# Optimization experiments

Hardware: AMD Instinct MI355X
Metric: run time of the kernel (lower is better)

## Reference

```python
import jax, jax.numpy as jnp
import numpy as np

N_NODES = 50000
N_EDGES = 640000
HID = 128


def _lin_params(key, out_dim, in_dim):
    kw, kb = jax.random.split(key)
    W = jax.random.normal(kw, (out_dim, in_dim), dtype=jnp.float32) * 0.02
    b = jax.random.normal(kb, (out_dim,), dtype=jnp.float32) * 0.02
    return W, b


def setup_inputs() -> dict:
    key = jax.random.key(0)
    ks = jax.random.split(key, 12)
    x = jax.random.normal(ks[0], (N_NODES, 3), dtype=jnp.float32)
    h = jax.random.normal(ks[1], (N_NODES, HID), dtype=jnp.float32)
    edge_index = jax.random.randint(ks[2], (2, N_EDGES), 0, N_NODES, dtype=jnp.int64)
    # edge_mlp: Linear(2H+1,H) -> SiLU -> Linear(H,H) -> SiLU -> Linear(H,H)
    ew1, eb1 = _lin_params(ks[3], HID, 2 * HID + 1)
    ew2, eb2 = _lin_params(ks[4], HID, HID)
    ew3, eb3 = _lin_params(ks[5], HID, HID)
    # coord_mlp: Linear(H,H) -> SiLU -> Linear(H,1)
    cw1, cb1 = _lin_params(ks[6], HID, HID)
    cw2, cb2 = _lin_params(ks[7], 1, HID)
    # node_mlp: Linear(2H,H) -> SiLU -> Linear(H,H) -> SiLU -> Linear(H,H)
    nw1, nb1 = _lin_params(ks[8], HID, 2 * HID)
    nw2, nb2 = _lin_params(ks[9], HID, HID)
    nw3, nb3 = _lin_params(ks[10], HID, HID)
    return {
        "x": x, "h": h, "edge_index": edge_index,
        "ew1": ew1, "eb1": eb1, "ew2": ew2, "eb2": eb2, "ew3": ew3, "eb3": eb3,
        "cw1": cw1, "cb1": cb1, "cw2": cw2, "cb2": cb2,
        "nw1": nw1, "nb1": nb1, "nw2": nw2, "nb2": nb2, "nw3": nw3, "nb3": nb3,
    }


def _lin(z, W, b):
    return z @ W.T + b


def _mlp3(z, W1, b1, W2, b2, W3, b3):
    z = jax.nn.silu(_lin(z, W1, b1))
    z = jax.nn.silu(_lin(z, W2, b2))
    return _lin(z, W3, b3)


def reference(x, h, edge_index,
              ew1, eb1, ew2, eb2, ew3, eb3,
              cw1, cb1, cw2, cb2,
              nw1, nb1, nw2, nb2, nw3, nb3):
    n = h.shape[0]
    src, dst = edge_index[0], edge_index[1]
    rel = x[src] - x[dst]                                   # [E, 3]
    d2 = jnp.sum(rel * rel, axis=-1, keepdims=True)         # [E, 1]
    e_in = jnp.concatenate([h[src], h[dst], d2], axis=-1)   # [E, 2H+1]
    m_ij = _mlp3(e_in, ew1, eb1, ew2, eb2, ew3, eb3)        # [E, H]
    m_aggr = jax.ops.segment_sum(m_ij, src, num_segments=n)  # [N, H]
    coord_coef = jnp.tanh(_lin(jax.nn.silu(_lin(m_ij, cw1, cb1)), cw2, cb2))  # [E, 1]
    delta_x = jax.ops.segment_sum(rel * coord_coef, src, num_segments=n)      # [N, 3]
    x_out = x + delta_x
    h_out = h + _mlp3(jnp.concatenate([h, m_aggr], axis=-1), nw1, nb1, nw2, nb2, nw3, nb3)
    return (x_out, h_out)
```

## Files before the change

### kernel.cpp

```cpp
#include <hip/hip_runtime.h>
#include <hip/hip_bf16.h>

#define N_NODES 50000
#define N_EDGES 640000
#define HID 128
#define EDG 128

typedef unsigned short ushort_t;
typedef __attribute__((ext_vector_type(8))) short bf16x8;
typedef __attribute__((ext_vector_type(4))) float f32x4;

#define U_MAGGR 0
#define U_HB    6400000
#define U_W1B   12800000
#define U_W2B   12832768
#define U_W3B   12849152
#define U_C1B   12865536
#define U_N1B   12881920
#define U_N2B   12914688
#define U_N3B   12931072
#define U_W1D2  12947456
#define U_WC    12947712
#define U_BC    12964096
#define U_SD    12964352
#define U_CNT   15524352
#define U_PTR   15624448

__device__ __forceinline__ float silu_f(float v) {
    const float e = __builtin_amdgcn_exp2f(v * -1.442695041f);
    return v * __builtin_amdgcn_rcpf(1.0f + e);
}

__device__ __forceinline__ ushort_t f2b(float f) {
    __hip_bfloat16 b = __float2bfloat16(f);
    return __builtin_bit_cast(ushort_t, b);
}
__device__ __forceinline__ float b2f(ushort_t u) {
    union { float f; unsigned int i; } v; v.i = ((unsigned int)u) << 16; return v.f;
}
__device__ __forceinline__ float u2f(unsigned int u) {
    union { float f; unsigned int i; } v; v.i = u; return v.f;
}
__device__ __forceinline__ unsigned int pack2(float a, float b) {
    return (unsigned int)f2b(a) | ((unsigned int)f2b(b) << 16);
}
__device__ __forceinline__ void up8(const uint4& u, float* f) {
    f[0] = u2f(u.x << 16); f[1] = u2f(u.x & 0xffff0000u);
    f[2] = u2f(u.y << 16); f[3] = u2f(u.y & 0xffff0000u);
    f[4] = u2f(u.z << 16); f[5] = u2f(u.z & 0xffff0000u);
    f[6] = u2f(u.w << 16); f[7] = u2f(u.w & 0xffff0000u);
}
__device__ __forceinline__ void atom_add_f32(float* p, float v) { unsafeAtomicAdd(p, v); }

__device__ __forceinline__ void atom_pk_bf16(ushort_t* p, unsigned int v) {
#if __has_builtin(__builtin_amdgcn_global_atomic_fadd_v2bf16)
    typedef __attribute__((ext_vector_type(2))) short s2;
    s2 sv = __builtin_bit_cast(s2, v);
    __builtin_amdgcn_global_atomic_fadd_v2bf16((__attribute__((address_space(1))) s2*)p, sv);
#else
    unsigned int* up = (unsigned int*)p;
    unsigned int old = __hip_atomic_load(up, __ATOMIC_RELAXED, __HIP_MEMORY_SCOPE_AGENT), assumed;
    do {
        assumed = old;
        float lo = b2f((ushort_t)(assumed & 0xffff)) + b2f((ushort_t)(v & 0xffff));
        float hi = b2f((ushort_t)(assumed >> 16)) + b2f((ushort_t)(v >> 16));
        unsigned int nv = (unsigned int)f2b(lo) | ((unsigned int)f2b(hi) << 16);
        old = atomicCAS(up, assumed, nv);
    } while (old != assumed);
#endif
}

__global__ void prep_kernel(const float* __restrict__ x, const float* __restrict__ h,
                            const float* __restrict__ ew1, const float* __restrict__ ew2,
                            const float* __restrict__ ew3, const float* __restrict__ cw1,
                            const float* __restrict__ nw1, const float* __restrict__ nw2,
                            const float* __restrict__ nw3, const int* __restrict__ ei,
                            ushort_t* __restrict__ wsu, float* __restrict__ xout) {
    long i = (long)blockIdx.x * 256 + threadIdx.x;
    if (i < 800000) {
        ((uint4*)(wsu + U_MAGGR))[i] = make_uint4(0u, 0u, 0u, 0u);
        return;
    }
    i -= 800000;
    if (i < 800000) {
        const float4* h4 = (const float4*)h;
        const float4 f0 = h4[2 * i], f1 = h4[2 * i + 1];
        ((uint4*)(wsu + U_HB))[i] = make_uint4(pack2(f0.x, f0.y), pack2(f0.z, f0.w),
                                               pack2(f1.x, f1.y), pack2(f1.z, f1.w));
        return;
    }
    i -= 800000;
    if (i < 32768) {
        const int f = (int)(i >> 7);
        const int k = (int)(i & 127);
        const int src = (f < 128) ? (f * 257 + k) : ((f - 128) * 257 + 128 + k);
        wsu[U_W1B + i] = f2b(ew1[src]);
        return;
    }
    i -= 32768;
    if (i < 16384) { wsu[U_W2B + i] = f2b(ew2[i]); return; }
    i -= 16384;
    if (i < 16384) { wsu[U_W3B + i] = f2b(ew3[i]); return; }
    i -= 16384;
    if (i < 16384) { wsu[U_C1B + i] = f2b(cw1[i]); return; }
    i -= 16384;
    if (i < 32768) { wsu[U_N1B + i] = f2b(nw1[i]); return; }
    i -= 32768;
    if (i < 16384) { wsu[U_N2B + i] = f2b(nw2[i]); return; }
    i -= 16384;
    if (i < 16384) { wsu[U_N3B + i] = f2b(nw3[i]); return; }
    i -= 16384;
    if (i < 128) { ((float*)(wsu + U_W1D2))[i] = ew1[i * 257 + 256]; return; }
    i -= 128;
    if (i < 37500) { ((float4*)xout)[i] = ((const float4*)x)[i]; return; }
    i -= 37500;
    if (i < N_EDGES) {
        atomicAdd(((unsigned int*)(wsu + U_CNT)) + ei[i], 1u);
    }
}

__global__ void scatter_kernel(const int* __restrict__ ei, unsigned int* __restrict__ ptr,
                               int2* __restrict__ sd) {
    const int e = blockIdx.x * 256 + threadIdx.x;
    if (e >= N_EDGES) return;
    const int s = ei[e], d = ei[N_EDGES + e];
    const unsigned int pos = atomicAdd(&ptr[s], 1u);
    sd[pos] = make_int2(s, d);
}

__global__ __launch_bounds__(256, 4) void ab_kernel(
    const ushort_t* __restrict__ hb, const ushort_t* __restrict__ wab,
    const float* __restrict__ eb1, ushort_t* __restrict__ abp,
    const ushort_t* __restrict__ c1b, const float* __restrict__ ew3,
    const float* __restrict__ eb3, const float* __restrict__ cb1,
    ushort_t* __restrict__ wcb, float* __restrict__ bcv,
    const unsigned int* __restrict__ cnt, unsigned int* __restrict__ ptr, int nAB) {
    __shared__ ushort_t sH[16384];
    const int t = threadIdx.x;
    const int lane = t & 63;
    const int wid = t >> 6;
    const int r15 = lane & 15;
    const int khi = lane >> 4;
    const int rhi = khi * 4;

    if ((int)blockIdx.x == nAB + 1) {
        __shared__ unsigned int sSum[256];
        const int lo = t * 196;
        const int hi = (lo + 196 < N_NODES) ? lo + 196 : N_NODES;
        unsigned int s = 0;
#pragma unroll 4
        for (int i = lo; i < hi; ++i) s += cnt[i];
        sSum[t] = s;
        __syncthreads();
#pragma unroll
        for (int off = 1; off < 256; off <<= 1) {
            const unsigned int v = (t >= off) ? sSum[t - off] : 0u;
            __syncthreads();
            sSum[t] += v;
            __syncthreads();
        }
        unsigned int run = (t == 0) ? 0u : sSum[t - 1];
#pragma unroll 4
        for (int i = lo; i < hi; ++i) { const unsigned int c = cnt[i]; ptr[i] = run; run += c; }
        return;
    }

    if ((int)blockIdx.x == nAB) {
        for (int i = t; i < 16384; i += 256) {
            const int m = i >> 7, k = i & 127;
            sH[(k * 128 + m) ^ ((k & 7) << 3)] = f2b(ew3[i]);
        }
        __syncthreads();
#pragma unroll
        for (int kh = 0; kh < 2; ++kh) {
#pragma unroll
            for (int fi = 0; fi < 2; ++fi) {
                const int f0 = wid * 32 + fi * 16;
                const int kc = kh * 64;
                f32x4 acc[4];
#pragma unroll
                for (int ni = 0; ni < 4; ++ni) acc[ni] = (f32x4){0.f, 0.f, 0.f, 0.f};
#pragma unroll
                for (int ks = 0; ks < 4; ++ks) {
                    const bf16x8 a0 = *(const bf16x8*)(c1b + (f0 + r15) * 128 + ks * 32 + khi * 8);
                    bf16x8 b[4];
#pragma unroll
                    for (int ni = 0; ni < 4; ++ni) {
                        const int kk = kc + ni * 16 + r15;
                        b[ni] = *(const bf16x8*)(sH + ((kk * 128 + ks * 32 + khi * 8) ^ ((kk & 7) << 3)));
                    }
#pragma unroll
                    for (int ni = 0; ni < 4; ++ni)
                        acc[ni] = __builtin_amdgcn_mfma_f32_16x16x32_bf16(a0, b[ni], acc[ni], 0, 0, 0);
                }
#pragma unroll
                for (int ni = 0; ni < 4; ++ni) {
                    const int kk = kc + ni * 16 + r15;
#pragma unroll
                    for (int j = 0; j < 4; ++j)
                        wcb[(f0 + rhi + j) * 128 + kk] = f2b(acc[ni][j]);
                }
            }
        }
        {
            const int f = t >> 1, hf = t & 1;
            float s = 0.f;
            const int m0 = hf * 64;
#pragma unroll 8
            for (int m = m0; m < m0 + 64; ++m)
                s = fmaf(b2f(c1b[f * 128 + m]), eb3[m], s);
            s += __shfl_xor(s, 1);
            if (hf == 0) bcv[f] = cb1[f] + s;
        }
        return;
    }

    const int fb = wid * 64;
    const int n0 = blockIdx.x * 64;

    const uint4* hb4 = (const uint4*)hb;
#pragma unroll
    for (int it = 0; it < 4; ++it) {
        const int idx = it * 256 + t;
        const int e = idx >> 4, c = idx & 15;
        const int n = n0 + e;
        uint4 v = make_uint4(0u, 0u, 0u, 0u);
        if (n < N_NODES) v = hb4[(size_t)n * 16 + c];
        const int ui = (e * 128 + c * 8) ^ ((e & 7) << 3);
        *(uint4*)(sH + ui) = v;
    }
    __syncthreads();

    f32x4 acc[4][4];
#pragma unroll
    for (int mi = 0; mi < 4; ++mi)
#pragma unroll
        for (int ni = 0; ni < 4; ++ni) acc[mi][ni] = (f32x4){0.f, 0.f, 0.f, 0.f};
#pragma unroll
    for (int ks = 0; ks < 4; ++ks) {
        bf16x8 a[4];
#pragma unroll
        for (int mi = 0; mi < 4; ++mi)
            a[mi] = *(const bf16x8*)(wab + (fb + mi * 16 + r15) * 128 + ks * 32 + khi * 8);
        bf16x8 b[4];
#pragma unroll
        for (int ni = 0; ni < 4; ++ni) {
            const int e = ni * 16 + r15;
            const int ui = (e * 128 + ks * 32 + khi * 8) ^ ((e & 7) << 3);
            b[ni] = *(const bf16x8*)(sH + ui);
        }
#pragma unroll
        for (int mi = 0; mi < 4; ++mi)
#pragma unroll
            for (int ni = 0; ni < 4; ++ni)
                acc[mi][ni] = __builtin_amdgcn_mfma_f32_16x16x32_bf16(a[mi], b[ni], acc[mi][ni], 0, 0, 0);
    }

#pragma unroll
    for (int mi = 0; mi < 4; ++mi) {
        const int f0 = fb + mi * 16 + rhi;
        float4 bb = make_float4(0.f, 0.f, 0.f, 0.f);
        if (f0 >= 128) bb = *(const float4*)&eb1[f0 - 128];
#pragma unroll
        for (int ni = 0; ni < 4; ++ni) {
            const int n = n0 + ni * 16 + r15;
            if (n < N_NODES) {
                *(uint2*)(abp + (size_t)n * 256 + f0) =
                    make_uint2(pack2(acc[mi][ni][0] + bb.x, acc[mi][ni][1] + bb.y),
                               pack2(acc[mi][ni][2] + bb.z, acc[mi][ni][3] + bb.w));
            }
        }
    }
}

template <bool ACT, int NE>
__device__ __forceinline__ void dense128(ushort_t* sE, int srcBase, int dstBase,
                                         const ushort_t* __restrict__ W,
                                         const float* __restrict__ bias,
                                         int r15, int khi, int rhi, int fb) {
    f32x4 acc[NE];
#pragma unroll
    for (int ni = 0; ni < NE; ++ni) acc[ni] = (f32x4){0.f, 0.f, 0.f, 0.f};
#pragma unroll
    for (int ks = 0; ks < 4; ++ks) {
        const bf16x8 a0 = *(const bf16x8*)(W + (fb + r15) * 128 + ks * 32 + khi * 8);
        bf16x8 b[NE];
#pragma unroll
        for (int ni = 0; ni < NE; ++ni) {
            const int edge = ni * 16 + r15;
            const int ui = (srcBase + edge * 128 + ks * 32 + khi * 8) ^ ((edge & 7) << 3);
            b[ni] = *(const bf16x8*)(sE + ui);
        }
#pragma unroll
        for (int ni = 0; ni < NE; ++ni)
            acc[ni] = __builtin_amdgcn_mfma_f32_16x16x32_bf16(a0, b[ni], acc[ni], 0, 0, 0);
    }
    const float4 bb = *(const float4*)&bias[fb + rhi];
#pragma unroll
    for (int ni = 0; ni < NE; ++ni) {
        const int edge = ni * 16 + r15;
        float v0 = acc[ni][0] + bb.x;
        float v1 = acc[ni][1] + bb.y;
        float v2 = acc[ni][2] + bb.z;
        float v3 = acc[ni][3] + bb.w;
        if (ACT) { v0 = silu_f(v0); v1 = silu_f(v1); v2 = silu_f(v2); v3 = silu_f(v3); }
        const int ui = (dstBase + edge * 128 + fb + rhi) ^ ((edge & 7) << 3);
        *(uint2*)(sE + ui) = make_uint2(pack2(v0, v1), pack2(v2, v3));
    }
}

__global__ __launch_bounds__(512, 4) void edge_kernel(
    const float* __restrict__ x, const ushort_t* __restrict__ ab,
    const int2* __restrict__ sd,
    const float* __restrict__ w1d2,
    const ushort_t* __restrict__ w2b, const float* __restrict__ eb2,
    const ushort_t* __restrict__ w3b, const float* __restrict__ eb3,
    const ushort_t* __restrict__ wcb, const float* __restrict__ bcv,
    const float* __restrict__ cw2, const float* __restrict__ cb2,
    float* __restrict__ xout, ushort_t* __restrict__ maggr) {
    __shared__ ushort_t sE[32768];
    __shared__ float srel[EDG][3];
    __shared__ float sd2[EDG];
    __shared__ int ssrc[EDG];
    __shared__ float sPart[8][EDG];

    const int t = threadIdx.x;
    const int lane = t & 63;
    const int wid = t >> 6;
    const int r15 = lane & 15;
    const int khi = lane >> 4;
    const int rhi = khi * 4;
    const int fb = wid * 16;
    const int e0 = blockIdx.x * EDG;

    uint4 va[4], vb[4];
    const int c = t & 15;
    const int ebase = t >> 4;
    {
        const uint4* ab4 = (const uint4*)ab;
#pragma unroll
        for (int it = 0; it < 4; ++it) {
            const int e = it * 32 + ebase;
            const int2 p = sd[e0 + e];
            va[it] = ab4[(size_t)p.x * 32 + c];
            vb[it] = ab4[(size_t)p.y * 32 + 16 + c];
        }
    }
    if (t < EDG) {
        const int2 p = sd[e0 + t];
        ssrc[t] = p.x;
        const float rx = x[3 * p.x] - x[3 * p.y];
        const float ry = x[3 * p.x + 1] - x[3 * p.y + 1];
        const float rz = x[3 * p.x + 2] - x[3 * p.y + 2];
        srel[t][0] = rx; srel[t][1] = ry; srel[t][2] = rz;
        sd2[t] = rx * rx + ry * ry + rz * rz;
    }
    __syncthreads();

    {
        const float4 w0 = *(const float4*)&w1d2[c * 8];
        const float4 w1 = *(const float4*)&w1d2[c * 8 + 4];
#pragma unroll
        for (int it = 0; it < 4; ++it) {
            const int e = it * 32 + ebase;
            const float d2 = sd2[e];
            float fa[8], fbv[8];
            up8(va[it], fa);
            up8(vb[it], fbv);
            const float v0 = silu_f(fmaf(d2, w0.x, fa[0] + fbv[0]));
            const float v1 = silu_f(fmaf(d2, w0.y, fa[1] + fbv[1]));
            const float v2 = silu_f(fmaf(d2, w0.z, fa[2] + fbv[2]));
            const float v3 = silu_f(fmaf(d2, w0.w, fa[3] + fbv[3]));
            const float v4 = silu_f(fmaf(d2, w1.x, fa[4] + fbv[4]));
            const float v5 = silu_f(fmaf(d2, w1.y, fa[5] + fbv[5]));
            const float v6 = silu_f(fmaf(d2, w1.z, fa[6] + fbv[6]));
            const float v7 = silu_f(fmaf(d2, w1.w, fa[7] + fbv[7]));
            uint4 st;
            st.x = pack2(v0, v1); st.y = pack2(v2, v3);
            st.z = pack2(v4, v5); st.w = pack2(v6, v7);
            *(uint4*)(sE + ((e * 128 + c * 8) ^ ((e & 7) << 3))) = st;
        }
    }
    __syncthreads();

    dense128<true, EDG / 16>(sE, 0, 16384, w2b, eb2, r15, khi, rhi, fb);
    __syncthreads();

    dense128<false, EDG / 16>(sE, 16384, 0, w3b, eb3, r15, khi, rhi, fb);

    {
        f32x4 acc[EDG / 16];
#pragma unroll
        for (int ni = 0; ni < EDG / 16; ++ni) acc[ni] = (f32x4){0.f, 0.f, 0.f, 0.f};
#pragma unroll
        for (int ks = 0; ks < 4; ++ks) {
            const bf16x8 a0 = *(const bf16x8*)(wcb + (fb + r15) * 128 + ks * 32 + khi * 8);
            bf16x8 b[EDG / 16];
#pragma unroll
            for (int ni = 0; ni < EDG / 16; ++ni) {
                const int edge = ni * 16 + r15;
                const int u = (16384 + edge * 128 + ks * 32 + khi * 8) ^ ((edge & 7) << 3);
                b[ni] = *(const bf16x8*)(sE + u);
            }
#pragma unroll
            for (int ni = 0; ni < EDG / 16; ++ni)
                acc[ni] = __builtin_amdgcn_mfma_f32_16x16x32_bf16(a0, b[ni], acc[ni], 0, 0, 0);
        }
        const float4 bb = *(const float4*)&bcv[fb + rhi];
        const float4 cw = *(const float4*)&cw2[fb + rhi];
        float p[EDG / 16];
#pragma unroll
        for (int ni = 0; ni < EDG / 16; ++ni) {
            float s = silu_f(acc[ni][0] + bb.x) * cw.x;
            s = fmaf(silu_f(acc[ni][1] + bb.y), cw.y, s);
            s = fmaf(silu_f(acc[ni][2] + bb.z), cw.z, s);
            s = fmaf(silu_f(acc[ni][3] + bb.w), cw.w, s);
            p[ni] = s;
        }
#pragma unroll
        for (int ni = 0; ni < EDG / 16; ++ni) {
            p[ni] += __shfl_xor(p[ni], 16);
            p[ni] += __shfl_xor(p[ni], 32);
        }
        if (khi == 0) {
#pragma unroll
            for (int ni = 0; ni < EDG / 16; ++ni) sPart[wid][ni * 16 + r15] = p[ni];
        }
    }
    __syncthreads();

    if (t < EDG) {
        float s = sPart[0][t];
#pragma unroll
        for (int w = 1; w < 8; ++w) s += sPart[w][t];
        const float coef = tanhf(s + cb2[0]);
        sPart[0][t] = srel[t][0] * coef;
        sPart[1][t] = srel[t][1] * coef;
        sPart[2][t] = srel[t][2] * coef;
    }

    {
        const int dw = t & 63;
        const int rs = t >> 6;
        float lo = 0.f, hi = 0.f;
        int cur = ssrc[rs * 16];
#pragma unroll
        for (int j = 0; j < 16; ++j) {
            const int e = rs * 16 + j;
            const int s = ssrc[e];
            if (s != cur) {
                atom_pk_bf16(maggr + (size_t)cur * 128 + dw * 2, pack2(lo, hi));
                lo = 0.f; hi = 0.f; cur = s;
            }
            const unsigned int v = *(const unsigned int*)(sE + ((e * 128 + dw * 2) ^ ((e & 7) << 3)));
            lo += b2f((ushort_t)(v & 0xffff));
            hi += b2f((ushort_t)(v >> 16));
        }
        atom_pk_bf16(maggr + (size_t)cur * 128 + dw * 2, pack2(lo, hi));
    }
    __syncthreads();

    if (t < EDG) {
        const bool last = (t == EDG - 1) || (ssrc[t + 1] != ssrc[t]);
        if (last) {
            const int s = ssrc[t];
            float ax = 0.f, ay = 0.f, az = 0.f;
            int j = t;
            while (j >= 0 && ssrc[j] == s) {
                ax += sPart[0][j]; ay += sPart[1][j]; az += sPart[2][j];
                --j;
            }
            atom_add_f32(&xout[3 * s + 0], ax);
            atom_add_f32(&xout[3 * s + 1], ay);
            atom_add_f32(&xout[3 * s + 2], az);
        }
    }
}

__global__ __launch_bounds__(256, 4) void node_kernel(
    const float* __restrict__ h, const ushort_t* __restrict__ hb,
    const ushort_t* __restrict__ maggr,
    const ushort_t* __restrict__ n1b, const float* __restrict__ nb1,
    const ushort_t* __restrict__ n2b, const float* __restrict__ nb2,
    const ushort_t* __restrict__ n3b, const float* __restrict__ nb3,
    float* __restrict__ hout) {
    __shared__ ushort_t sE[16384];
    const int t = threadIdx.x;
    const int lane = t & 63;
    const int wid = t >> 6;
    const int r15 = lane & 15;
    const int khi = lane >> 4;
    const int rhi = khi * 4;
    const int fb = wid * 32;
    const int n0 = blockIdx.x * 64;

    const uint4* hb4 = (const uint4*)hb;
    const uint4* mg4 = (const uint4*)maggr;
#pragma unroll
    for (int it = 0; it < 8; ++it) {
        const int idx = it * 256 + t;
        const int e = idx >> 5, c = idx & 31;
        const int n = n0 + e;
        uint4 v = make_uint4(0u, 0u, 0u, 0u);
        if (n < N_NODES) v = (c < 16) ? hb4[(size_t)n * 16 + c] : mg4[(size_t)n * 16 + (c - 16)];
        const int ui = (e * 256 + c * 8) ^ ((e & 7) << 3);
        *(uint4*)(sE + ui) = v;
    }
    __syncthreads();

    f32x4 acc[2][4];
#pragma unroll
    for (int mi = 0; mi < 2; ++mi)
#pragma unroll
        for (int ni = 0; ni < 4; ++ni) acc[mi][ni] = (f32x4){0.f, 0.f, 0.f, 0.f};
#pragma unroll
    for (int ks = 0; ks < 8; ++ks) {
        const bf16x8 a0 = *(const bf16x8*)(n1b + (fb + r15) * 256 + ks * 32 + khi * 8);
        const bf16x8 a1 = *(const bf16x8*)(n1b + (fb + 16 + r15) * 256 + ks * 32 + khi * 8);
        bf16x8 b[4];
#pragma unroll
        for (int ni = 0; ni < 4; ++ni) {
            const int edge = ni * 16 + r15;
            const int ui = (edge * 256 + ks * 32 + khi * 8) ^ ((edge & 7) << 3);
            b[ni] = *(const bf16x8*)(sE + ui);
        }
#pragma unroll
        for (int ni = 0; ni < 4; ++ni) {
            acc[0][ni] = __builtin_amdgcn_mfma_f32_16x16x32_bf16(a0, b[ni], acc[0][ni], 0, 0, 0);
            acc[1][ni] = __builtin_amdgcn_mfma_f32_16x16x32_bf16(a1, b[ni], acc[1][ni], 0, 0, 0);
        }
    }
    __syncthreads();
    {
        const float4 bb0 = *(const float4*)&nb1[fb + rhi];
        const float4 bb1 = *(const float4*)&nb1[fb + 16 + rhi];
#pragma unroll
        for (int mi = 0; mi < 2; ++mi) {
            const float4 bb = mi ? bb1 : bb0;
#pragma unroll
            for (int ni = 0; ni < 4; ++ni) {
                const int edge = ni * 16 + r15;
                const float v0 = silu_f(acc[mi][ni][0] + bb.x);
                const float v1 = silu_f(acc[mi][ni][1] + bb.y);
                const float v2 = silu_f(acc[mi][ni][2] + bb.z);
                const float v3 = silu_f(acc[mi][ni][3] + bb.w);
                const int ui = (edge * 128 + fb + mi * 16 + rhi) ^ ((edge & 7) << 3);
                *(uint2*)(sE + ui) = make_uint2(pack2(v0, v1), pack2(v2, v3));
            }
        }
    }
    __syncthreads();

    {
#pragma unroll
        for (int half = 0; half < 2; ++half) {
            f32x4 a2[4];
#pragma unroll
            for (int ni = 0; ni < 4; ++ni) a2[ni] = (f32x4){0.f, 0.f, 0.f, 0.f};
            const int fbh = fb + half * 16;
#pragma unroll
            for (int ks = 0; ks < 4; ++ks) {
                const bf16x8 a0 = *(const bf16x8*)(n2b + (fbh + r15) * 128 + ks * 32 + khi * 8);
                bf16x8 b[4];
#pragma unroll
                for (int ni = 0; ni < 4; ++ni) {
                    const int edge = ni * 16 + r15;
                    const int ui = (edge * 128 + ks * 32 + khi * 8) ^ ((edge & 7) << 3);
                    b[ni] = *(const bf16x8*)(sE + ui);
                }
#pragma unroll
                for (int ni = 0; ni < 4; ++ni)
                    a2[ni] = __builtin_amdgcn_mfma_f32_16x16x32_bf16(a0, b[ni], a2[ni], 0, 0, 0);
            }
            const float4 bb = *(const float4*)&nb2[fbh + rhi];
#pragma unroll
            for (int ni = 0; ni < 4; ++ni) {
                const int edge = ni * 16 + r15;
                const float v0 = silu_f(a2[ni][0] + bb.x);
                const float v1 = silu_f(a2[ni][1] + bb.y);
                const float v2 = silu_f(a2[ni][2] + bb.z);
                const float v3 = silu_f(a2[ni][3] + bb.w);
                const int ui = (8192 + edge * 128 + fbh + rhi) ^ ((edge & 7) << 3);
                *(uint2*)(sE + ui) = make_uint2(pack2(v0, v1), pack2(v2, v3));
            }
        }
    }
    __syncthreads();

    {
        f32x4 a3[2][4];
#pragma unroll
        for (int mi = 0; mi < 2; ++mi)
#pragma unroll
            for (int ni = 0; ni < 4; ++ni) a3[mi][ni] = (f32x4){0.f, 0.f, 0.f, 0.f};
#pragma unroll
        for (int ks = 0; ks < 4; ++ks) {
            const bf16x8 a0 = *(const bf16x8*)(n3b + (fb + r15) * 128 + ks * 32 + khi * 8);
            const bf16x8 a1 = *(const bf16x8*)(n3b + (fb + 16 + r15) * 128 + ks * 32 + khi * 8);
            bf16x8 b[4];
#pragma unroll
            for (int ni = 0; ni < 4; ++ni) {
                const int edge = ni * 16 + r15;
                const int ui = (8192 + edge * 128 + ks * 32 + khi * 8) ^ ((edge & 7) << 3);
                b[ni] = *(const bf16x8*)(sE + ui);
            }
#pragma unroll
            for (int ni = 0; ni < 4; ++ni) {
                a3[0][ni] = __builtin_amdgcn_mfma_f32_16x16x32_bf16(a0, b[ni], a3[0][ni], 0, 0, 0);
                a3[1][ni] = __builtin_amdgcn_mfma_f32_16x16x32_bf16(a1, b[ni], a3[1][ni], 0, 0, 0);
            }
        }
        const float4 bb0 = *(const float4*)&nb3[fb + rhi];
        const float4 bb1 = *(const float4*)&nb3[fb + 16 + rhi];
#pragma unroll
        for (int mi = 0; mi < 2; ++mi) {
            const float4 bb = mi ? bb1 : bb0;
#pragma unroll
            for (int ni = 0; ni < 4; ++ni) {
                const int n = n0 + ni * 16 + r15;
                if (n < N_NODES) {
                    const size_t o = (size_t)n * 128 + fb + mi * 16 + rhi;
                    const float4 hv = *(const float4*)&h[o];
                    float4 ov;
                    ov.x = hv.x + a3[mi][ni][0] + bb.x;
                    ov.y = hv.y + a3[mi][ni][1] + bb.y;
                    ov.z = hv.z + a3[mi][ni][2] + bb.z;
                    ov.w = hv.w + a3[mi][ni][3] + bb.w;
                    *(float4*)&hout[o] = ov;
                }
            }
        }
    }
}

extern "C" void kernel_launch(void* const* d_in, const int* in_sizes, int n_in,
                              void* d_out, int out_size, void* d_ws, size_t ws_size,
                              hipStream_t stream) {
    const float* x   = (const float*)d_in[0];
    const float* h   = (const float*)d_in[1];
    const int*   ei  = (const int*)d_in[2];
    const float* ew1 = (const float*)d_in[3];
    const float* eb1 = (const float*)d_in[4];
    const float* ew2 = (const float*)d_in[5];
    const float* eb2 = (const float*)d_in[6];
    const float* ew3 = (const float*)d_in[7];
    const float* eb3 = (const float*)d_in[8];
    const float* cw1 = (const float*)d_in[9];
    const float* cb1 = (const float*)d_in[10];
    const float* cw2 = (const float*)d_in[11];
    const float* cb2 = (const float*)d_in[12];
    const float* nw1 = (const float*)d_in[13];
    const float* nb1 = (const float*)d_in[14];
    const float* nw2 = (const float*)d_in[15];
    const float* nb2 = (const float*)d_in[16];
    const float* nw3 = (const float*)d_in[17];
    const float* nb3 = (const float*)d_in[18];

    float* out  = (float*)d_out;
    float* xout = out;
    float* hout = out + (size_t)N_NODES * 3;
    ushort_t* wsu = (ushort_t*)d_ws;

    ushort_t* maggr = wsu + U_MAGGR;
    const ushort_t* hb  = wsu + U_HB;
    const ushort_t* wab = wsu + U_W1B;
    const ushort_t* w2b = wsu + U_W2B;
    const ushort_t* w3b = wsu + U_W3B;
    const ushort_t* c1b = wsu + U_C1B;
    const ushort_t* n1b = wsu + U_N1B;
    const ushort_t* n2b = wsu + U_N2B;
    const ushort_t* n3b = wsu + U_N3B;
    const float* w1d2 = (const float*)(wsu + U_W1D2);
    ushort_t* wcb = wsu + U_WC;
    float* bcv = (float*)(wsu + U_BC);
    int2* sd = (int2*)(wsu + U_SD);
    unsigned int* cnt = (unsigned int*)(wsu + U_CNT);
    unsigned int* ptr = (unsigned int*)(wsu + U_PTR);

    ushort_t* abp = (ushort_t*)hout;

    hipMemsetAsync(cnt, 0, 50048 * sizeof(unsigned int), stream);

    const long prep_total = 800000L + 800000L + 32768 + 3 * 16384 + 32768 + 2 * 16384 + 128 + 37500 + N_EDGES;
    const int prep_blocks = (int)((prep_total + 255) / 256);
    prep_kernel<<<prep_blocks, 256, 0, stream>>>(x, h, ew1, ew2, ew3, cw1, nw1, nw2, nw3,
                                                 ei, wsu, xout);

    const int nAB = (N_NODES + 63) / 64;
    ab_kernel<<<nAB + 2, 256, 0, stream>>>(hb, wab, eb1, abp,
                                           c1b, ew3, eb3, cb1, wcb, bcv,
                                           cnt, ptr, nAB);

    scatter_kernel<<<(N_EDGES + 255) / 256, 256, 0, stream>>>(ei, ptr, sd);

    edge_kernel<<<N_EDGES / EDG, 512, 0, stream>>>(x, abp, sd,
                                                   w1d2, w2b, eb2, w3b, eb3,
                                                   wcb, bcv, cw2, cb2,
                                                   xout, maggr);

    node_kernel<<<(N_NODES + 63) / 64, 256, 0, stream>>>(h, hb, maggr,
                                                         n1b, nb1, n2b, nb2, n3b, nb3,
                                                         hout);
}
```

Baseline: 321.2 us.

## Retile edge MLP to 32x64 warp tiles and fuse scatter into AB kernel

The edge kernel's dense layers now give each warp a 32-feature by 64-edge tile instead of a 16-feature by 128-edge tile. Each B fragment read from LDS then feeds two MFMAs, which halves LDS traffic per MFMA, and the coord partial sums reduce over 4 slots instead of 8. Separately, the prefix scan moves into its own 1024-thread kernel. The edge scatter runs as extra blocks of the AB GEMM kernel, which removes a launch and lets the scatter overlap with the GEMM. The costs are a serial single-block scan launch beforehand and higher register pressure per warp.

```diff
diff --git a/kernel.cpp b/kernel.cpp
--- a/kernel.cpp
+++ b/kernel.cpp
@@ -119,51 +119,53 @@
     }
 }
 
-__global__ void scatter_kernel(const int* __restrict__ ei, unsigned int* __restrict__ ptr,
-                               int2* __restrict__ sd) {
-    const int e = blockIdx.x * 256 + threadIdx.x;
-    if (e >= N_EDGES) return;
-    const int s = ei[e], d = ei[N_EDGES + e];
-    const unsigned int pos = atomicAdd(&ptr[s], 1u);
-    sd[pos] = make_int2(s, d);
-}
-
-__global__ __launch_bounds__(256, 4) void ab_kernel(
+__global__ __launch_bounds__(1024) void scan_kernel(const unsigned int* __restrict__ cnt,
+                                                    unsigned int* __restrict__ ptr) {
+    __shared__ unsigned int sSum[1024];
+    const int t = threadIdx.x;
+    const int lo = t * 49;
+    const int hi = (lo + 49 < N_NODES) ? lo + 49 : N_NODES;
+    unsigned int s = 0;
+    for (int i = lo; i < hi; ++i) s += cnt[i];
+    sSum[t] = s;
+    __syncthreads();
+#pragma unroll
+    for (int off = 1; off < 1024; off <<= 1) {
+        const unsigned int v = (t >= off) ? sSum[t - off] : 0u;
+        __syncthreads();
+        sSum[t] += v;
+        __syncthreads();
+    }
+    unsigned int run = (t == 0) ? 0u : sSum[t - 1];
+    for (int i = lo; i < hi; ++i) { const unsigned int c = cnt[i]; ptr[i] = run; run += c; }
+}
+
+__global__ __launch_bounds__(256, 4) void abscatter_kernel(
     const ushort_t* __restrict__ hb, const ushort_t* __restrict__ wab,
     const float* __restrict__ eb1, ushort_t* __restrict__ abp,
     const ushort_t* __restrict__ c1b, const float* __restrict__ ew3,
     const float* __restrict__ eb3, const float* __restrict__ cb1,
     ushort_t* __restrict__ wcb, float* __restrict__ bcv,
-    const unsigned int* __restrict__ cnt, unsigned int* __restrict__ ptr, int nAB) {
+    const int* __restrict__ ei, unsigned int* __restrict__ ptr, int2* __restrict__ sd,
+    int nAB) {
     __shared__ ushort_t sH[16384];
     const int t = threadIdx.x;
+
+    if ((int)blockIdx.x > nAB) {
+        const int e = ((int)blockIdx.x - nAB - 1) * 256 + t;
+        if (e < N_EDGES) {
+            const int s = ei[e], d = ei[N_EDGES + e];
+            const unsigned int pos = atomicAdd(&ptr[s], 1u);
+            sd[pos] = make_int2(s, d);
+        }
+        return;
+    }
+
     const int lane = t & 63;
     const int wid = t >> 6;
     const int r15 = lane & 15;
     const int khi = lane >> 4;
     const int rhi = khi * 4;
-
-    if ((int)blockIdx.x == nAB + 1) {
-        __shared__ unsigned int sSum[256];
-        const int lo = t * 196;
-        const int hi = (lo + 196 < N_NODES) ? lo + 196 : N_NODES;
-        unsigned int s = 0;
-#pragma unroll 4
-        for (int i = lo; i < hi; ++i) s += cnt[i];
-        sSum[t] = s;
-        __syncthreads();
-#pragma unroll
-        for (int off = 1; off < 256; off <<= 1) {
-            const unsigned int v = (t >= off) ? sSum[t - off] : 0u;
-            __syncthreads();
-            sSum[t] += v;
-            __syncthreads();
-        }
-        unsigned int run = (t == 0) ? 0u : sSum[t - 1];
-#pragma unroll 4
-        for (int i = lo; i < hi; ++i) { const unsigned int c = cnt[i]; ptr[i] = run; run += c; }
-        return;
-    }
 
     if ((int)blockIdx.x == nAB) {
         for (int i = t; i < 16384; i += 256) {
@@ -273,39 +275,49 @@
     }
 }
 
-template <bool ACT, int NE>
-__device__ __forceinline__ void dense128(ushort_t* sE, int srcBase, int dstBase,
-                                         const ushort_t* __restrict__ W,
-                                         const float* __restrict__ bias,
-                                         int r15, int khi, int rhi, int fb) {
-    f32x4 acc[NE];
-#pragma unroll
-    for (int ni = 0; ni < NE; ++ni) acc[ni] = (f32x4){0.f, 0.f, 0.f, 0.f};
+template <bool ACT>
+__device__ __forceinline__ void dense32x64(ushort_t* sE, int srcBase, int dstBase,
+                                           const ushort_t* __restrict__ W,
+                                           const float* __restrict__ bias,
+                                           int r15, int khi, int rhi, int fb, int eb) {
+    f32x4 acc[2][4];
+#pragma unroll
+    for (int mi = 0; mi < 2; ++mi)
+#pragma unroll
+        for (int ni = 0; ni < 4; ++ni) acc[mi][ni] = (f32x4){0.f, 0.f, 0.f, 0.f};
 #pragma unroll
     for (int ks = 0; ks < 4; ++ks) {
         const bf16x8 a0 = *(const bf16x8*)(W + (fb + r15) * 128 + ks * 32 + khi * 8);
-        bf16x8 b[NE];
-#pragma unroll
-        for (int ni = 0; ni < NE; ++ni) {
-            const int edge = ni * 16 + r15;
+        const bf16x8 a1 = *(const bf16x8*)(W + (fb + 16 + r15) * 128 + ks * 32 + khi * 8);
+        bf16x8 b[4];
+#pragma unroll
+        for (int ni = 0; ni < 4; ++ni) {
+            const int edge = eb + ni * 16 + r15;
             const int ui = (srcBase + edge * 128 + ks * 32 + khi * 8) ^ ((edge & 7) << 3);
             b[ni] = *(const bf16x8*)(sE + ui);
         }
 #pragma unroll
-        for (int ni = 0; ni < NE; ++ni)
-            acc[ni] = __builtin_amdgcn_mfma_f32_16x16x32_bf16(a0, b[ni], acc[ni], 0, 0, 0);
-    }
-    const float4 bb = *(const float4*)&bias[fb + rhi];
-#pragma unroll
-    for (int ni = 0; ni < NE; ++ni) {
-        const int edge = ni * 16 + r15;
-        float v0 = acc[ni][0] + bb.x;
-        float v1 = acc[ni][1] + bb.y;
-        float v2 = acc[ni][2] + bb.z;
-        float v3 = acc[ni][3] + bb.w;
-        if (ACT) { v0 = silu_f(v0); v1 = silu_f(v1); v2 = silu_f(v2); v3 = silu_f(v3); }
-        const int ui = (dstBase + edge * 128 + fb + rhi) ^ ((edge & 7) << 3);
-        *(uint2*)(sE + ui) = make_uint2(pack2(v0, v1), pack2(v2, v3));
+        for (int ni = 0; ni < 4; ++ni) {
+            acc[0][ni] = __builtin_amdgcn_mfma_f32_16x16x32_bf16(a0, b[ni], acc[0][ni], 0, 0, 0);
+            acc[1][ni] = __builtin_amdgcn_mfma_f32_16x16x32_bf16(a1, b[ni], acc[1][ni], 0, 0, 0);
+        }
+    }
+    const float4 bb0 = *(const float4*)&bias[fb + rhi];
+    const float4 bb1 = *(const float4*)&bias[fb + 16 + rhi];
+#pragma unroll
+    for (int mi = 0; mi < 2; ++mi) {
+        const float4 bb = mi ? bb1 : bb0;
+#pragma unroll
+        for (int ni = 0; ni < 4; ++ni) {
+            const int edge = eb + ni * 16 + r15;
+            float v0 = acc[mi][ni][0] + bb.x;
+            float v1 = acc[mi][ni][1] + bb.y;
+            float v2 = acc[mi][ni][2] + bb.z;
+            float v3 = acc[mi][ni][3] + bb.w;
+            if (ACT) { v0 = silu_f(v0); v1 = silu_f(v1); v2 = silu_f(v2); v3 = silu_f(v3); }
+            const int ui = (dstBase + edge * 128 + fb + mi * 16 + rhi) ^ ((edge & 7) << 3);
+            *(uint2*)(sE + ui) = make_uint2(pack2(v0, v1), pack2(v2, v3));
+        }
     }
 }
 
@@ -322,7 +334,7 @@
     __shared__ float srel[EDG][3];
     __shared__ float sd2[EDG];
     __shared__ int ssrc[EDG];
-    __shared__ float sPart[8][EDG];
+    __shared__ float sPart[4][EDG];
 
     const int t = threadIdx.x;
     const int lane = t & 63;
@@ -330,7 +342,10 @@
     const int r15 = lane & 15;
     const int khi = lane >> 4;
     const int rhi = khi * 4;
-    const int fb = wid * 16;
+    const int fg = wid & 3;
+    const int eh = wid >> 2;
+    const int fb = fg * 32;
+    const int eb = eh * 64;
     const int e0 = blockIdx.x * EDG;
 
     uint4 va[4], vb[4];
@@ -383,56 +398,65 @@
     }
     __syncthreads();
 
-    dense128<true, EDG / 16>(sE, 0, 16384, w2b, eb2, r15, khi, rhi, fb);
-    __syncthreads();
-
-    dense128<false, EDG / 16>(sE, 16384, 0, w3b, eb3, r15, khi, rhi, fb);
+    dense32x64<true>(sE, 0, 16384, w2b, eb2, r15, khi, rhi, fb, eb);
+    __syncthreads();
+
+    dense32x64<false>(sE, 16384, 0, w3b, eb3, r15, khi, rhi, fb, eb);
 
     {
-        f32x4 acc[EDG / 16];
-#pragma unroll
-        for (int ni = 0; ni < EDG / 16; ++ni) acc[ni] = (f32x4){0.f, 0.f, 0.f, 0.f};
+        f32x4 acc[2][4];
+#pragma unroll
+        for (int mi = 0; mi < 2; ++mi)
+#pragma unroll
+            for (int ni = 0; ni < 4; ++ni) acc[mi][ni] = (f32x4){0.f, 0.f, 0.f, 0.f};
 #pragma unroll
         for (int ks = 0; ks < 4; ++ks) {
             const bf16x8 a0 = *(const bf16x8*)(wcb + (fb + r15) * 128 + ks * 32 + khi * 8);
-            bf16x8 b[EDG / 16];
-#pragma unroll
-            for (int ni = 0; ni < EDG / 16; ++ni) {
-                const int edge = ni * 16 + r15;
+            const bf16x8 a1 = *(const bf16x8*)(wcb + (fb + 16 + r15) * 128 + ks * 32 + khi * 8);
+            bf16x8 b[4];
+#pragma unroll
+            for (int ni = 0; ni < 4; ++ni) {
+                const int edge = eb + ni * 16 + r15;
                 const int u = (16384 + edge * 128 + ks * 32 + khi * 8) ^ ((edge & 7) << 3);
                 b[ni] = *(const bf16x8*)(sE + u);
             }
 #pragma unroll
-            for (int ni = 0; ni < EDG / 16; ++ni)
-                acc[ni] = __builtin_amdgcn_mfma_f32_16x16x32_bf16(a0, b[ni], acc[ni], 0, 0, 0);
-        }
-        const float4 bb = *(const float4*)&bcv[fb + rhi];
-        const float4 cw = *(const float4*)&cw2[fb + rhi];
-        float p[EDG / 16];
-#pragma unroll
-        for (int ni = 0; ni < EDG / 16; ++ni) {
-            float s = silu_f(acc[ni][0] + bb.x) * cw.x;
-            s = fmaf(silu_f(acc[ni][1] + bb.y), cw.y, s);
-            s = fmaf(silu_f(acc[ni][2] + bb.z), cw.z, s);
-            s = fmaf(silu_f(acc[ni][3] + bb.w), cw.w, s);
+            for (int ni = 0; ni < 4; ++ni) {
+                acc[0][ni] = __builtin_amdgcn_mfma_f32_16x16x32_bf16(a0, b[ni], acc[0][ni], 0, 0, 0);
+                acc[1][ni] = __builtin_amdgcn_mfma_f32_16x16x32_bf16(a1, b[ni], acc[1][ni], 0, 0, 0);
+            }
+        }
+        const float4 bb0 = *(const float4*)&bcv[fb + rhi];
+        const float4 bb1 = *(const float4*)&bcv[fb + 16 + rhi];
+        const float4 cw0 = *(const float4*)&cw2[fb + rhi];
+        const float4 cw1v = *(const float4*)&cw2[fb + 16 + rhi];
+        float p[4];
+#pragma unroll
+        for (int ni = 0; ni < 4; ++ni) {
+            float s = silu_f(acc[0][ni][0] + bb0.x) * cw0.x;
+            s = fmaf(silu_f(acc[0][ni][1] + bb0.y), cw0.y, s);
+            s = fmaf(silu_f(acc[0][ni][2] + bb0.z), cw0.z, s);
+            s = fmaf(silu_f(acc[0][ni][3] + bb0.w), cw0.w, s);
+            s = fmaf(silu_f(acc[1][ni][0] + bb1.x), cw1v.x, s);
+            s = fmaf(silu_f(acc[1][ni][1] + bb1.y), cw1v.y, s);
+            s = fmaf(silu_f(acc[1][ni][2] + bb1.z), cw1v.z, s);
+            s = fmaf(silu_f(acc[1][ni][3] + bb1.w), cw1v.w, s);
             p[ni] = s;
         }
 #pragma unroll
-        for (int ni = 0; ni < EDG / 16; ++ni) {
+        for (int ni = 0; ni < 4; ++ni) {
             p[ni] += __shfl_xor(p[ni], 16);
             p[ni] += __shfl_xor(p[ni], 32);
         }
         if (khi == 0) {
 #pragma unroll
-            for (int ni = 0; ni < EDG / 16; ++ni) sPart[wid][ni * 16 + r15] = p[ni];
+            for (int ni = 0; ni < 4; ++ni) sPart[fg][eb + ni * 16 + r15] = p[ni];
         }
     }
     __syncthreads();
 
     if (t < EDG) {
-        float s = sPart[0][t];
-#pragma unroll
-        for (int w = 1; w < 8; ++w) s += sPart[w][t];
+        const float s = sPart[0][t] + sPart[1][t] + sPart[2][t] + sPart[3][t];
         const float coef = tanhf(s + cb2[0]);
         sPart[0][t] = srel[t][0] * coef;
         sPart[1][t] = srel[t][1] * coef;
@@ -686,12 +710,13 @@
     prep_kernel<<<prep_blocks, 256, 0, stream>>>(x, h, ew1, ew2, ew3, cw1, nw1, nw2, nw3,
                                                  ei, wsu, xout);
 
+    scan_kernel<<<1, 1024, 0, stream>>>(cnt, ptr);
+
     const int nAB = (N_NODES + 63) / 64;
-    ab_kernel<<<nAB + 2, 256, 0, stream>>>(hb, wab, eb1, abp,
-                                           c1b, ew3, eb3, cb1, wcb, bcv,
-                                           cnt, ptr, nAB);
-
-    scatter_kernel<<<(N_EDGES + 255) / 256, 256, 0, stream>>>(ei, ptr, sd);
+    const int nSC = (N_EDGES + 255) / 256;
+    abscatter_kernel<<<nAB + 1 + nSC, 256, 0, stream>>>(hb, wab, eb1, abp,
+                                                        c1b, ew3, eb3, cb1, wcb, bcv,
+                                                        ei, ptr, sd, nAB);
 
     edge_kernel<<<N_EDGES / EDG, 512, 0, stream>>>(x, abp, sd,
                                                    w1d2, w2b, eb2, w3b, eb3,
```

Result: slower. 400.5 us (+24.7%).
